# Kernel optimization log

Measured on AMD Instinct MI355X. Metric: run time of the kernel, lower is better.

The kernel has to match this reference:

```python
import jax, jax.numpy as jnp
import numpy as np

SIGMA = 1.0
LN2 = 0.6931471805599453


def _raster_mask(kd, kh, kw, include_center):
    # PixelCNN-style causal mask in (depth, h, w) raster order
    idx = np.arange(kd * kh * kw).reshape(kd, kh, kw)
    c = (kd * kh * kw) // 2
    m = (idx <= c) if include_center else (idx < c)
    return jnp.asarray(m, jnp.float32)[None, None]  # [1,1,kd,kh,kw] (OIDHW broadcast)


def _conv3d(x, w, b, padding):
    y = jax.lax.conv_general_dilated(x, w, (1, 1, 1), padding,
                                     dimension_numbers=('NCDHW', 'OIDHW', 'NCDHW'))
    return y + b[None, :, None, None, None]


def _quantize1d(x, centers):
    # distances of every element to every center: [..., L]
    d = (x[..., None] - centers) ** 2
    phi_soft = jax.nn.softmax(-SIGMA * d, axis=-1)
    qsoft = jnp.einsum('...l,l->...', phi_soft, centers)
    symbols = jnp.argmin(d, axis=-1)  # int32 hard assignment
    qhard = centers[symbols]
    return qsoft, qhard, symbols


def setup_inputs() -> dict:
    key = jax.random.key(0)
    ks = jax.random.split(key, 8)
    N, H, W, C = 4, 128, 128, 16
    K, L = 24, 6
    s = 0.05
    return {
        'x': jax.random.normal(ks[0], (N, H, W, C), jnp.float32),
        'centers': jax.random.uniform(ks[1], (L,), jnp.float32, -2.0, 2.0),
        'w0': jax.random.normal(ks[2], (K, 1, 3, 3, 3), jnp.float32) * s,
        'b0': jnp.zeros((K,), jnp.float32),
        'w1': jax.random.normal(ks[3], (K, K, 3, 3, 3), jnp.float32) * s,
        'b1': jnp.zeros((K,), jnp.float32),
        'w2': jax.random.normal(ks[4], (K, K, 3, 3, 3), jnp.float32) * s,
        'b2': jnp.zeros((K,), jnp.float32),
        'w_out': jax.random.normal(ks[5], (L, K, 1, 1, 1), jnp.float32) * s,
        'b_out': jnp.zeros((L,), jnp.float32),
    }


def reference(x, centers, w0, b0, w1, b1, w2, b2, w_out, b_out):
    # ---- soft/hard quantization with straight-through estimator ----
    qsoft, qhard, symbols = _quantize1d(x, centers)
    qbar = qsoft + jax.lax.stop_gradient(qhard - qsoft)  # [N,H,W,C] NHWC

    pc_in = jnp.transpose(qbar, (0, 3, 1, 2))[:, None]      # [N,1,C,H,W] (depth=C)
    tgt = jnp.transpose(symbols, (0, 3, 1, 2))              # [N,C,H,W]

    # pad input volume with pad_value = centers[0] (causal boundary symbol)
    pad_value = centers[0].astype(pc_in.dtype)
    v = jax.lax.pad(pc_in, pad_value,
                    [(0, 0, 0), (0, 0, 0), (1, 1, 0), (1, 1, 0), (1, 1, 0)])

    mask_a = _raster_mask(3, 3, 3, include_center=False)
    mask_b = _raster_mask(3, 3, 3, include_center=True)

    # res_shallow: masked-A conv -> masked-B conv -> masked-B conv + residual -> 1x1x1 logits
    h0 = jax.nn.relu(_conv3d(v, w0 * mask_a, b0, 'VALID'))     # [N,K,C,H,W]
    h1 = jax.nn.relu(_conv3d(h0, w1 * mask_b, b1, 'SAME'))
    h2 = _conv3d(h1, w2 * mask_b, b2, 'SAME') + h0
    logits = _conv3d(jax.nn.relu(h2), w_out, b_out, 'SAME')    # [N,L,C,H,W]

    # per-element bitcost: cross-entropy of hard symbols, in bits
    lp = jax.nn.log_softmax(logits, axis=1)
    bc = -jnp.take_along_axis(lp, tgt[:, None], axis=1)[:, 0] / LN2  # [N,C,H,W]
    bc_train = jnp.transpose(bc, (0, 2, 3, 1))                        # NCHW -> NHWC
    return qbar, bc_train
```

## Files before the change

kernel.cpp:

```cpp
#include <hip/hip_runtime.h>
#include <cstddef>

typedef _Float16 f16;
typedef _Float16 f16x8 __attribute__((ext_vector_type(8)));
typedef float f32x16 __attribute__((ext_vector_type(16)));

#define N_ 4
#define D_ 16
#define H_ 128
#define W_ 128
#define K_ 24
#define L_ 6
#define NTAP_A 13

#define OFF_Q    0ull
#define OFF_TGT  4194304ull
#define OFF_H0   8388608ull
#define OFF_H1   58720256ull
#define OFF_W0P  109051904ull
#define OFF_W1B  109053952ull
#define OFF_W2B  109075456ull

#define AROW_B 6336
#define A_BYTES 120384
#define B_BYTES 21504
#define SMEM_BYTES 141888

__host__ __device__ constexpr int aoff(int p, int c, int g) {
  int idx8 = 2 * c + g;
  int ts = idx8 >= 3 ? 1 : 0;
  int t = 2 * p + ts;
  int cb = idx8 - 3 * ts;
  int dz = t / 9 - 1;
  int rr = t % 9;
  int dy = rr / 3 - 1;
  int dx = rr % 3 - 1;
  int rowb = (dz < 0) ? (dy + 1) : (10 + dy + 1);
  return rowb * AROW_B + (dx + 1) * 48 + cb * 16;
}

__global__ void pack_weights_k(const float* __restrict__ w0,
                               const float* __restrict__ w1,
                               const float* __restrict__ w2,
                               float* __restrict__ w0p,
                               f16* __restrict__ w1B,
                               f16* __restrict__ w2B) {
  int gid = blockIdx.x * 256 + threadIdx.x;
  for (int i = gid; i < NTAP_A * K_; i += 2048) {
    int co = i % K_;
    int t  = i / K_;
    w0p[t * K_ + co] = w0[co * 27 + t];
  }
  for (int i = gid; i < 2 * 10752; i += 2048) {
    int sel = i / 10752;
    int idx = i % 10752;
    int chunk = idx / 512;
    int r = idx % 512;
    int g = r / 256;
    int n = (r % 256) / 8;
    int j = r % 8;
    int p = chunk / 3, c = chunk % 3;
    int idx8 = 2 * c + g;
    int ts = idx8 >= 3 ? 1 : 0;
    int t = 2 * p + ts;
    int ci = (idx8 - 3 * ts) * 8 + j;
    const float* w = sel ? w2 : w1;
    float v = (n < K_) ? w[(n * K_ + ci) * 27 + t] : 0.f;
    (sel ? w2B : w1B)[idx] = (f16)v;
  }
}

__global__ __launch_bounds__(256) void quantize_k(
    const float* __restrict__ x, const float* __restrict__ centers,
    float* __restrict__ qbar_out, float* __restrict__ q,
    int* __restrict__ tgt) {
  int idx = blockIdx.x * 256 + threadIdx.x;
  int w = idx & 127;
  int h = (idx >> 7) & 127;
  int c = (idx >> 14) & 15;
  int n = idx >> 18;

  float cs[L_];
#pragma unroll
  for (int l = 0; l < L_; ++l) cs[l] = centers[l];

  int xi = ((n * H_ + h) * W_ + w) * D_ + c;
  float xv = x[xi];

  float dv[L_];
  float dmin = 3.4e38f;
  int sym = 0;
#pragma unroll
  for (int l = 0; l < L_; ++l) {
    float df = xv - cs[l];
    float d = df * df;
    dv[l] = d;
    if (d < dmin) { dmin = d; sym = l; }
  }
  float e[L_];
  float s = 0.f;
#pragma unroll
  for (int l = 0; l < L_; ++l) {
    e[l] = expf(dmin - dv[l]);
    s += e[l];
  }
  float qsoft = 0.f;
#pragma unroll
  for (int l = 0; l < L_; ++l) qsoft += (e[l] / s) * cs[l];

  float qhard = cs[sym];
  float qb = qsoft + (qhard - qsoft);

  qbar_out[xi] = qb;
  q[idx] = qb;
  tgt[idx] = sym;
}

__global__ __launch_bounds__(256) void conv0_k(
    const float* __restrict__ q, const float* __restrict__ w0p,
    const float* __restrict__ b0, const float* __restrict__ centers,
    f16* __restrict__ h0) {
  float pv = centers[0];

  int blk = blockIdx.x;
  int h2 = blk & 63;
  int d = (blk >> 6) & 15;
  int n = blk >> 10;
  int w = threadIdx.x & 127;
  int h = (h2 << 1) | (threadIdx.x >> 7);

  float acc[K_];
#pragma unroll
  for (int i = 0; i < K_; ++i) acc[i] = b0[i];

  const float* base = q + ((n * D_ + d) * H_ + h) * W_ + w;

#pragma unroll 1
  for (int t = 0; t < NTAP_A; ++t) {
    int dz = t / 9 - 1;
    int r = t % 9;
    int dy = r / 3 - 1;
    int dx = r % 3 - 1;
    int hh = h + dy, ww = w + dx, dd = d + dz;
    bool ok = (dd >= 0) && ((unsigned)hh < H_) && ((unsigned)ww < W_);
    float xv = ok ? base[(dz * H_ + dy) * W_ + dx] : pv;
    const float* wr = w0p + t * K_;
#pragma unroll
    for (int co = 0; co < K_; ++co) acc[co] = fmaf(xv, wr[co], acc[co]);
  }

  union { f16 hv[24]; uint4 u[3]; } u;
#pragma unroll
  for (int i = 0; i < K_; ++i) u.hv[i] = (f16)fmaxf(acc[i], 0.f);
  size_t pos = (size_t)(((n * D_ + d) * H_ + h) * W_ + w);
  uint4* dst = (uint4*)(h0 + pos * K_);
  dst[0] = u.u[0]; dst[1] = u.u[1]; dst[2] = u.u[2];
}

__device__ __forceinline__ void conv_core8(const f16* __restrict__ src,
                                           const f16* __restrict__ wB,
                                           char* smem, int n, int d, int h_base,
                                           f32x16& acc0, f32x16& acc1) {
  const int tid = threadIdx.x;
  for (int i = tid; i < 7296; i += 1024) {
    int r = i / 384, qq = i % 384;
    int dd = (r < 10) ? d - 1 : d;
    int hh = h_base - 1 + ((r < 10) ? r : r - 10);
    uint4 v = make_uint4(0, 0, 0, 0);
    if (dd >= 0 && (unsigned)hh < (unsigned)H_)
      v = ((const uint4*)(src + (size_t)((n * D_ + dd) * H_ + hh) * 3072))[qq];
    *(uint4*)(smem + r * AROW_B + 48 + qq * 16) = v;
  }
  if (tid < 114) {
    int r = tid / 6, k = tid % 6;
    int byte = r * AROW_B + (k < 3 ? k * 16 : 6192 + (k - 3) * 16);
    *(uint4*)(smem + byte) = make_uint4(0, 0, 0, 0);
  }
  {
    const uint4* g = (const uint4*)wB;
    uint4* s = (uint4*)(smem + A_BYTES);
    for (int i = tid; i < 1344; i += 1024) s[i] = g[i];
  }
  __syncthreads();

  const int lane = tid & 63;
  const int wv = tid >> 6;
  const int m = lane & 31;
  const int g01 = lane >> 5;

  const int hs = wv >> 1;
  const int wc0 = (wv & 1) * 64;
  const char* Ab0 = smem + hs * AROW_B + (wc0 + m) * 48;
  const char* Ab1 = Ab0 + 32 * 48;
  const char* Bb = smem + A_BYTES + g01 * 512 + m * 16;

#pragma unroll
  for (int r = 0; r < 16; ++r) { acc0[r] = 0.f; acc1[r] = 0.f; }

#pragma unroll
  for (int p = 0; p < 7; ++p) {
#pragma unroll
    for (int c = 0; c < 3; ++c) {
      const int C0 = aoff(p, c, 0);
      const int C1 = aoff(p, c, 1);
      int off = g01 ? C1 : C0;
      f16x8 b = *(const f16x8*)(Bb + (p * 3 + c) * 1024);
      f16x8 a0 = *(const f16x8*)(Ab0 + off);
      f16x8 a1 = *(const f16x8*)(Ab1 + off);
      acc0 = __builtin_amdgcn_mfma_f32_32x32x16_f16(a0, b, acc0, 0, 0, 0);
      acc1 = __builtin_amdgcn_mfma_f32_32x32x16_f16(a1, b, acc1, 0, 0, 0);
    }
  }
}

__global__ __launch_bounds__(1024, 1) void conv1_mfma_k(
    const f16* __restrict__ src, const f16* __restrict__ wB,
    const float* __restrict__ bias, f16* __restrict__ dst) {
  __shared__ __align__(16) char smem[SMEM_BYTES];

  int blk = blockIdx.x;
  int hb = blk & 15;
  int d = (blk >> 4) & 15;
  int n = blk >> 8;
  int h_base = hb * 8;

  f32x16 acc0, acc1;
  conv_core8(src, wB, smem, n, d, h_base, acc0, acc1);

  const int lane = threadIdx.x & 63;
  const int wv = threadIdx.x >> 6;
  const int m = lane & 31;
  const int g01 = lane >> 5;

  __syncthreads();
  f16* ldsE = (f16*)smem;
  if (m < K_) {
    float bv = bias[m];
#pragma unroll
    for (int tt = 0; tt < 2; ++tt) {
      const f32x16& A = tt ? acc1 : acc0;
#pragma unroll
      for (int r = 0; r < 16; ++r) {
        int mrow = (r & 3) + 8 * (r >> 2) + 4 * g01;
        int pos = (2 * wv + tt) * 32 + mrow;
        ldsE[pos * K_ + m] = (f16)fmaxf(A[r] + bv, 0.f);
      }
    }
  }
  __syncthreads();
  {
    uint4* g = (uint4*)(dst + (size_t)((n * D_ + d) * H_ + h_base) * 3072);
    const uint4* s = (const uint4*)smem;
    for (int i = threadIdx.x; i < 3072; i += 1024) g[i] = s[i];
  }
}

__global__ __launch_bounds__(1024, 1) void conv2_mfma_k(
    const f16* __restrict__ h1, const f16* __restrict__ h0,
    const f16* __restrict__ wB, const float* __restrict__ bias,
    const float* __restrict__ w_out, const float* __restrict__ b_out,
    const int* __restrict__ tgt, float* __restrict__ bco) {
  __shared__ __align__(16) char smem[SMEM_BYTES];

  int blk = blockIdx.x;
  int hb = blk & 15;
  int d = (blk >> 4) & 15;
  int n = blk >> 8;
  int h_base = hb * 8;

  f32x16 acc0, acc1;
  conv_core8(h1, wB, smem, n, d, h_base, acc0, acc1);

  const int lane = threadIdx.x & 63;
  const int wv = threadIdx.x >> 6;
  const int m = lane & 31;
  const int g01 = lane >> 5;

  __syncthreads();
  float* Ef = (float*)smem;
  if (m < K_) {
    float bv = bias[m];
#pragma unroll
    for (int tt = 0; tt < 2; ++tt) {
      const f32x16& A = tt ? acc1 : acc0;
#pragma unroll
      for (int r = 0; r < 16; ++r) {
        int mrow = (r & 3) + 8 * (r >> 2) + 4 * g01;
        int pos = (2 * wv + tt) * 32 + mrow;
        Ef[pos * 28 + m] = A[r] + bv;
      }
    }
  }
  __syncthreads();

  {
    int pos = threadIdx.x;
    int hh = h_base + (pos >> 7);
    int w = pos & 127;

    size_t gpos = (size_t)((n * D_ + d) * H_ + h_base) * W_ + pos;
    const f16x8* hp = (const f16x8*)(h0 + gpos * K_);
    f16x8 e0 = hp[0], e1 = hp[1], e2 = hp[2];

    const float* ef = Ef + pos * 28;
    float vals[K_];
#pragma unroll
    for (int k = 0; k < K_; ++k) {
      float h0v = (float)(k < 8 ? e0[k] : (k < 16 ? e1[k - 8] : e2[k - 16]));
      vals[k] = fmaxf(ef[k] + h0v, 0.f);
    }

    float lg[L_];
#pragma unroll
    for (int l = 0; l < L_; ++l) lg[l] = b_out[l];
#pragma unroll
    for (int k = 0; k < K_; ++k) {
      float rv = vals[k];
#pragma unroll
      for (int l = 0; l < L_; ++l) lg[l] = fmaf(rv, w_out[l * K_ + k], lg[l]);
    }
    float mm = lg[0];
#pragma unroll
    for (int l = 1; l < L_; ++l) mm = fmaxf(mm, lg[l]);
    float s = 0.f;
#pragma unroll
    for (int l = 0; l < L_; ++l) s += expf(lg[l] - mm);

    int t = tgt[gpos];
    float lt = lg[0];
#pragma unroll
    for (int l = 1; l < L_; ++l) lt = (t == l) ? lg[l] : lt;

    float lp = lt - mm - logf(s);
    bco[(size_t)((n * H_ + hh) * W_ + w) * D_ + d] = -lp / 0.69314718055994530942f;
  }
}

extern "C" void kernel_launch(void* const* d_in, const int* in_sizes, int n_in,
                              void* d_out, int out_size, void* d_ws, size_t ws_size,
                              hipStream_t stream) {
  const float* x       = (const float*)d_in[0];
  const float* centers = (const float*)d_in[1];
  const float* w0      = (const float*)d_in[2];
  const float* b0      = (const float*)d_in[3];
  const float* w1      = (const float*)d_in[4];
  const float* b1      = (const float*)d_in[5];
  const float* w2      = (const float*)d_in[6];
  const float* b2      = (const float*)d_in[7];
  const float* w_out   = (const float*)d_in[8];
  const float* b_out   = (const float*)d_in[9];
  float* out = (float*)d_out;

  char* ws = (char*)d_ws;
  float* q    = (float*)(ws + OFF_Q);
  int*   tg   = (int*)(ws + OFF_TGT);
  f16*   h0f  = (f16*)(ws + OFF_H0);
  f16*   h1f  = (f16*)(ws + OFF_H1);
  float* w0p  = (float*)(ws + OFF_W0P);
  f16*   w1B  = (f16*)(ws + OFF_W1B);
  f16*   w2B  = (f16*)(ws + OFF_W2B);

  hipLaunchKernelGGL(pack_weights_k, dim3(8), dim3(256), 0, stream,
                     w0, w1, w2, w0p, w1B, w2B);
  hipLaunchKernelGGL(quantize_k, dim3(4096), dim3(256), 0, stream,
                     x, centers, out, q, tg);
  hipLaunchKernelGGL(conv0_k, dim3(4096), dim3(256), 0, stream,
                     q, w0p, b0, centers, h0f);
  hipLaunchKernelGGL(conv1_mfma_k, dim3(1024), dim3(1024), 0, stream,
                     h0f, w1B, b1, h1f);
  hipLaunchKernelGGL(conv2_mfma_k, dim3(1024), dim3(1024), 0, stream,
                     h1f, h0f, w2B, b2, w_out, b_out, tg, out + 1048576);
}
```

Baseline: 197.7 us.

## Fuse quantization into conv0 with LDS halo tile and merge weight packing

Weight packing is merged into the qbar kernel, which now writes qbar in NHWC directly without the intermediate NCHW q buffer. Conv0 now recomputes quantization for its halo tile from x into shared memory, writes the target symbols, and stages its fp16 outputs in LDS for coalesced stores. This removes one launch and the round trip of the q buffer through global memory. In exchange, quantization is recomputed for halo rows and x is read with a stride of D_ floats in conv0.

Result: slower. 207.3 us (+4.9%).

```diff
diff --git a/kernel.cpp b/kernel.cpp
--- a/kernel.cpp
+++ b/kernel.cpp
@@ -13,13 +13,12 @@
 #define L_ 6
 #define NTAP_A 13
 
-#define OFF_Q    0ull
-#define OFF_TGT  4194304ull
-#define OFF_H0   8388608ull
-#define OFF_H1   58720256ull
-#define OFF_W0P  109051904ull
-#define OFF_W1B  109053952ull
-#define OFF_W2B  109075456ull
+#define OFF_TGT  0ull
+#define OFF_H0   4194304ull
+#define OFF_H1   54525952ull
+#define OFF_W0P  104857600ull
+#define OFF_W1B  104858880ull
+#define OFF_W2B  104880384ull
 
 #define AROW_B 6336
 #define A_BYTES 120384
@@ -39,57 +38,11 @@
   return rowb * AROW_B + (dx + 1) * 48 + cb * 16;
 }
 
-__global__ void pack_weights_k(const float* __restrict__ w0,
-                               const float* __restrict__ w1,
-                               const float* __restrict__ w2,
-                               float* __restrict__ w0p,
-                               f16* __restrict__ w1B,
-                               f16* __restrict__ w2B) {
-  int gid = blockIdx.x * 256 + threadIdx.x;
-  for (int i = gid; i < NTAP_A * K_; i += 2048) {
-    int co = i % K_;
-    int t  = i / K_;
-    w0p[t * K_ + co] = w0[co * 27 + t];
-  }
-  for (int i = gid; i < 2 * 10752; i += 2048) {
-    int sel = i / 10752;
-    int idx = i % 10752;
-    int chunk = idx / 512;
-    int r = idx % 512;
-    int g = r / 256;
-    int n = (r % 256) / 8;
-    int j = r % 8;
-    int p = chunk / 3, c = chunk % 3;
-    int idx8 = 2 * c + g;
-    int ts = idx8 >= 3 ? 1 : 0;
-    int t = 2 * p + ts;
-    int ci = (idx8 - 3 * ts) * 8 + j;
-    const float* w = sel ? w2 : w1;
-    float v = (n < K_) ? w[(n * K_ + ci) * 27 + t] : 0.f;
-    (sel ? w2B : w1B)[idx] = (f16)v;
-  }
-}
-
-__global__ __launch_bounds__(256) void quantize_k(
-    const float* __restrict__ x, const float* __restrict__ centers,
-    float* __restrict__ qbar_out, float* __restrict__ q,
-    int* __restrict__ tgt) {
-  int idx = blockIdx.x * 256 + threadIdx.x;
-  int w = idx & 127;
-  int h = (idx >> 7) & 127;
-  int c = (idx >> 14) & 15;
-  int n = idx >> 18;
-
-  float cs[L_];
-#pragma unroll
-  for (int l = 0; l < L_; ++l) cs[l] = centers[l];
-
-  int xi = ((n * H_ + h) * W_ + w) * D_ + c;
-  float xv = x[xi];
-
+__device__ __forceinline__ void quant1(float xv, const float cs[L_],
+                                       float& qb, int& sym) {
   float dv[L_];
   float dmin = 3.4e38f;
-  int sym = 0;
+  sym = 0;
 #pragma unroll
   for (int l = 0; l < L_; ++l) {
     float df = xv - cs[l];
@@ -107,54 +60,128 @@
   float qsoft = 0.f;
 #pragma unroll
   for (int l = 0; l < L_; ++l) qsoft += (e[l] / s) * cs[l];
-
-  float qhard = cs[sym];
-  float qb = qsoft + (qhard - qsoft);
-
-  qbar_out[xi] = qb;
-  q[idx] = qb;
-  tgt[idx] = sym;
-}
-
-__global__ __launch_bounds__(256) void conv0_k(
-    const float* __restrict__ q, const float* __restrict__ w0p,
-    const float* __restrict__ b0, const float* __restrict__ centers,
-    f16* __restrict__ h0) {
-  float pv = centers[0];
+  qb = qsoft + (cs[sym] - qsoft);
+}
+
+__global__ __launch_bounds__(256) void qbar_pack_k(
+    const float* __restrict__ x, const float* __restrict__ centers,
+    float* __restrict__ qbar_out,
+    const float* __restrict__ w0, const float* __restrict__ w1,
+    const float* __restrict__ w2, float* __restrict__ w0p,
+    f16* __restrict__ w1B, f16* __restrict__ w2B) {
+  int idx = blockIdx.x * 256 + threadIdx.x;
+
+  float cs[L_];
+#pragma unroll
+  for (int l = 0; l < L_; ++l) cs[l] = centers[l];
+
+  float qb; int sym;
+  quant1(x[idx], cs, qb, sym);
+  qbar_out[idx] = qb;
+
+  if (blockIdx.x < 8) {
+    int gid = blockIdx.x * 256 + threadIdx.x;
+    for (int i = gid; i < NTAP_A * K_; i += 2048) {
+      int co = i % K_;
+      int t  = i / K_;
+      w0p[t * K_ + co] = w0[co * 27 + t];
+    }
+    for (int i = gid; i < 2 * 10752; i += 2048) {
+      int sel = i / 10752;
+      int idx2 = i % 10752;
+      int chunk = idx2 / 512;
+      int r = idx2 % 512;
+      int g = r / 256;
+      int nn = (r % 256) / 8;
+      int j = r % 8;
+      int p = chunk / 3, c = chunk % 3;
+      int idx8 = 2 * c + g;
+      int ts = idx8 >= 3 ? 1 : 0;
+      int t = 2 * p + ts;
+      int ci = (idx8 - 3 * ts) * 8 + j;
+      const float* w = sel ? w2 : w1;
+      float v = (nn < K_) ? w[(nn * K_ + ci) * 27 + t] : 0.f;
+      (sel ? w2B : w1B)[idx2] = (f16)v;
+    }
+  }
+}
+
+__global__ __launch_bounds__(256, 2) void conv0_fused_k(
+    const float* __restrict__ x, const float* __restrict__ centers,
+    const float* __restrict__ w0p, const float* __restrict__ b0,
+    f16* __restrict__ h0, int* __restrict__ tgt) {
+  __shared__ float qs[19 * 132];
+  __shared__ f16 eo[1024 * K_];
 
   int blk = blockIdx.x;
-  int h2 = blk & 63;
-  int d = (blk >> 6) & 15;
-  int n = blk >> 10;
-  int w = threadIdx.x & 127;
-  int h = (h2 << 1) | (threadIdx.x >> 7);
-
-  float acc[K_];
-#pragma unroll
-  for (int i = 0; i < K_; ++i) acc[i] = b0[i];
-
-  const float* base = q + ((n * D_ + d) * H_ + h) * W_ + w;
+  int hb = blk & 15;
+  int d = (blk >> 4) & 15;
+  int n = blk >> 8;
+  int h_base = hb * 8;
+
+  float cs[L_];
+#pragma unroll
+  for (int l = 0; l < L_; ++l) cs[l] = centers[l];
+  float pv = cs[0];
+
+  for (int i = threadIdx.x; i < 19 * 130; i += 256) {
+    int r = i / 130, s = i % 130;
+    int dd = (r < 10) ? d - 1 : d;
+    int hh = h_base - 1 + ((r < 10) ? r : r - 10);
+    int ww = s - 1;
+    float qv = pv;
+    int sym = 0;
+    bool in = (dd >= 0) && ((unsigned)hh < (unsigned)H_) &&
+              ((unsigned)ww < (unsigned)W_);
+    if (in) {
+      float xv = x[((n * H_ + hh) * W_ + ww) * D_ + dd];
+      quant1(xv, cs, qv, sym);
+    }
+    qs[r * 132 + s] = qv;
+    if (r >= 11 && (unsigned)ww < (unsigned)W_)
+      tgt[((n * D_ + d) * H_ + (h_base + r - 11)) * W_ + ww] = sym;
+  }
+  __syncthreads();
+
+  float bia[K_];
+#pragma unroll
+  for (int co = 0; co < K_; ++co) bia[co] = b0[co];
 
 #pragma unroll 1
-  for (int t = 0; t < NTAP_A; ++t) {
-    int dz = t / 9 - 1;
-    int r = t % 9;
-    int dy = r / 3 - 1;
-    int dx = r % 3 - 1;
-    int hh = h + dy, ww = w + dx, dd = d + dz;
-    bool ok = (dd >= 0) && ((unsigned)hh < H_) && ((unsigned)ww < W_);
-    float xv = ok ? base[(dz * H_ + dy) * W_ + dx] : pv;
-    const float* wr = w0p + t * K_;
-#pragma unroll
-    for (int co = 0; co < K_; ++co) acc[co] = fmaf(xv, wr[co], acc[co]);
-  }
-
-  union { f16 hv[24]; uint4 u[3]; } u;
-#pragma unroll
-  for (int i = 0; i < K_; ++i) u.hv[i] = (f16)fmaxf(acc[i], 0.f);
-  size_t pos = (size_t)(((n * D_ + d) * H_ + h) * W_ + w);
-  uint4* dst = (uint4*)(h0 + pos * K_);
-  dst[0] = u.u[0]; dst[1] = u.u[1]; dst[2] = u.u[2];
+  for (int k = 0; k < 4; ++k) {
+    int p = threadIdx.x + 256 * k;
+    int rl = p >> 7;
+    int wl = p & 127;
+
+    float acc[K_];
+#pragma unroll
+    for (int co = 0; co < K_; ++co) acc[co] = bia[co];
+
+#pragma unroll
+    for (int t = 0; t < NTAP_A; ++t) {
+      int r, s;
+      if (t < 9)       { r = rl + t / 3; s = wl + t % 3; }
+      else if (t < 12) { r = rl + 10;    s = wl + (t - 9); }
+      else             { r = rl + 11;    s = wl; }
+      float xv = qs[r * 132 + s];
+      const float* wr = w0p + t * K_;
+#pragma unroll
+      for (int co = 0; co < K_; ++co) acc[co] = fmaf(xv, wr[co], acc[co]);
+    }
+
+    union { f16 hv[K_]; uint4 u[3]; } u;
+#pragma unroll
+    for (int co = 0; co < K_; ++co) u.hv[co] = (f16)fmaxf(acc[co], 0.f);
+    uint4* ep = (uint4*)(eo + p * K_);
+    ep[0] = u.u[0]; ep[1] = u.u[1]; ep[2] = u.u[2];
+  }
+  __syncthreads();
+
+  {
+    uint4* g = (uint4*)(h0 + (size_t)((n * D_ + d) * H_ + h_base) * (W_ * K_));
+    const uint4* s = (const uint4*)eo;
+    for (int i = threadIdx.x; i < 3072; i += 256) g[i] = s[i];
+  }
 }
 
 __device__ __forceinline__ void conv_core8(const f16* __restrict__ src,
@@ -352,7 +379,6 @@
   float* out = (float*)d_out;
 
   char* ws = (char*)d_ws;
-  float* q    = (float*)(ws + OFF_Q);
   int*   tg   = (int*)(ws + OFF_TGT);
   f16*   h0f  = (f16*)(ws + OFF_H0);
   f16*   h1f  = (f16*)(ws + OFF_H1);
@@ -360,12 +386,10 @@
   f16*   w1B  = (f16*)(ws + OFF_W1B);
   f16*   w2B  = (f16*)(ws + OFF_W2B);
 
-  hipLaunchKernelGGL(pack_weights_k, dim3(8), dim3(256), 0, stream,
-                     w0, w1, w2, w0p, w1B, w2B);
-  hipLaunchKernelGGL(quantize_k, dim3(4096), dim3(256), 0, stream,
-                     x, centers, out, q, tg);
-  hipLaunchKernelGGL(conv0_k, dim3(4096), dim3(256), 0, stream,
-                     q, w0p, b0, centers, h0f);
+  hipLaunchKernelGGL(qbar_pack_k, dim3(4096), dim3(256), 0, stream,
+                     x, centers, out, w0, w1, w2, w0p, w1B, w2B);
+  hipLaunchKernelGGL(conv0_fused_k, dim3(1024), dim3(256), 0, stream,
+                     x, centers, w0p, b0, h0f, tg);
   hipLaunchKernelGGL(conv1_mfma_k, dim3(1024), dim3(1024), 0, stream,
                      h0f, w1B, b1, h1f);
   hipLaunchKernelGGL(conv2_mfma_k, dim3(1024), dim3(1024), 0, stream,
```
